# Optimization experiments

Measured on AMD Instinct MI355X. Metric: run time of the kernel, lower is better.

The kernel has to match this reference:

```python
import jax, jax.numpy as jnp
import numpy as np

N_HEAD = 16
N_EMBD = 1024
BLOCK = 2048
B, T = 4, 2048


def setup_inputs() -> dict:
    key = jax.random.key(0)
    ks = jax.random.split(key, 5)
    s = 0.02
    return {
        "x": jax.random.normal(ks[0], (B, T, N_EMBD), dtype=jnp.float32),
        "qkv_w": jax.random.normal(ks[1], (3 * N_EMBD, N_EMBD), dtype=jnp.float32) * s,
        "qkv_b": jnp.zeros((3 * N_EMBD,), dtype=jnp.float32),
        "proj_w": jax.random.normal(ks[2], (N_EMBD, N_EMBD), dtype=jnp.float32) * s,
        "proj_b": jnp.zeros((N_EMBD,), dtype=jnp.float32),
    }


def reference(x, qkv_w, qkv_b, proj_w, proj_b):
    Bx, Tx, C = x.shape
    hd = C // N_HEAD
    qkv = x @ qkv_w.T + qkv_b  # [B,T,3C]
    q, k, v = jnp.split(qkv, 3, axis=-1)
    # [B,T,C] -> [B,H,T,hd]
    def heads(t):
        return t.reshape(Bx, Tx, N_HEAD, hd).transpose(0, 2, 1, 3)
    q, k, v = heads(q), heads(k), heads(v)
    scores = jnp.einsum("bhqd,bhkd->bhqk", q, k) / jnp.sqrt(jnp.float32(hd))
    causal = jnp.tril(jnp.ones((Tx, Tx), dtype=bool))
    scores = jnp.where(causal[None, None, :, :], scores, -jnp.inf)
    attn = jax.nn.softmax(scores, axis=-1)
    out = jnp.einsum("bhqk,bhkd->bhqd", attn, v)
    out = out.transpose(0, 2, 1, 3).reshape(Bx, Tx, C)
    return out @ proj_w.T + proj_b
```

## Files before the change

kernel.cpp:

```cpp
#include <hip/hip_runtime.h>
#include <stdint.h>
#include <math.h>

#define DEVI __device__ __forceinline__

typedef __attribute__((ext_vector_type(8))) short bf16x8;
typedef __attribute__((ext_vector_type(4))) float f32x4;

DEVI unsigned short f2bf(float f) {
  union { float f; unsigned u; } v; v.f = f;
  unsigned u = v.u;
  u += 0x7fffu + ((u >> 16) & 1u);
  return (unsigned short)(u >> 16);
}

DEVI unsigned cvt_pk_bf16(float a, float b) {
  unsigned r;
  asm("v_cvt_pk_bf16_f32 %0, %1, %2" : "=v"(r) : "v"(a), "v"(b));
  return r;
}

DEVI f32x4 mfma16(bf16x8 a, bf16x8 b, f32x4 c) {
  return __builtin_amdgcn_mfma_f32_16x16x32_bf16(a, b, c, 0, 0, 0);
}

DEVI void gld16(const unsigned short* g, unsigned short* l) {
  __builtin_amdgcn_global_load_lds(
      (const __attribute__((address_space(1))) unsigned int*)(uintptr_t)g,
      (__attribute__((address_space(3))) unsigned int*)(unsigned int)(uintptr_t)l,
      16, 0, 0);
}

#define VMCNT(n) asm volatile("s_waitcnt vmcnt(" #n ")" ::: "memory")
#define BAR()                              \
  do {                                     \
    __builtin_amdgcn_s_barrier();          \
    __builtin_amdgcn_sched_barrier(0);     \
  } while (0)

__global__ __launch_bounds__(256) void cvt_kernel(const float* __restrict__ in,
                                                  unsigned short* __restrict__ out, int n) {
  int i = (blockIdx.x * 256 + threadIdx.x) * 4;
  if (i < n) {
    float4 v = *(const float4*)(in + i);
    unsigned lo = f2bf(v.x) | ((unsigned)f2bf(v.y) << 16);
    unsigned hi = f2bf(v.z) | ((unsigned)f2bf(v.w) << 16);
    uint2 o; o.x = lo; o.y = hi;
    *(uint2*)(out + i) = o;
  }
}

template <int MODE>
__global__ __launch_bounds__(512, 2) void gemm8(
    const unsigned short* __restrict__ A, const unsigned short* __restrict__ Bw,
    const float* __restrict__ bias, float* __restrict__ Cf,
    unsigned short* __restrict__ Qo, unsigned short* __restrict__ Ko,
    unsigned short* __restrict__ Vo, int M, int N, int K, int nbx) {
  extern __shared__ unsigned short lds[];
  const int tid = threadIdx.x;
  const int lane = tid & 63;
  const int w = tid >> 6;
  const int wm = w >> 2, wn = w & 3;
  const int lr = lane & 15, lq = lane >> 4;

  const int cpx = gridDim.x >> 3;
  const int swz = (blockIdx.x & 7) * cpx + (blockIdx.x >> 3);
  const int bx = swz % nbx, by = swz / nbx;
  const int m0 = by * 256, n0 = bx * 256;

  const int sr = lane >> 3;
  const int sc = ((lane & 7) ^ sr) << 3;
  const unsigned short* pa = A + (size_t)(m0 + sr) * K + sc;
  const unsigned short* pb = Bw + (size_t)(n0 + sr) * K + sc;

  const int aA0 = w, aA1 = 16 + w;
  const int aB0 = 8 + w, aB1 = 24 + w;
  const int bA0 = (w & 3) + ((w >> 2) << 3), bA1 = bA0 + 16;
  const int bB0 = bA0 + 4, bB1 = bA1 + 4;

  const int bs0 = (lq ^ (lr & 7)) << 3;
  const int bs1 = ((lq + 4) ^ (lr & 7)) << 3;

  f32x4 acc[8][4] = {};

  auto sA = [&](int buf, int kt, int c) {
    gld16(pa + (size_t)(c << 3) * K + kt, lds + buf * 32768 + (c << 9));
  };
  auto sB = [&](int buf, int kt, int c) {
    gld16(pb + (size_t)(c << 3) * K + kt, lds + buf * 32768 + 16384 + (c << 9));
  };

#define PH(buf, mh, nh)                                                          \
  {                                                                              \
    const unsigned short* As_ = lds + (buf) * 32768;                             \
    const unsigned short* Bs_ = As_ + 16384;                                     \
    bf16x8 a0[4], a1[4], b0[2], b1[2];                                           \
    _Pragma("unroll") for (int i = 0; i < 4; ++i) {                              \
      int ar = wm * 128 + (mh) * 64 + i * 16 + lr;                               \
      a0[i] = *(const bf16x8*)(As_ + ar * 64 + bs0);                             \
      a1[i] = *(const bf16x8*)(As_ + ar * 64 + bs1);                             \
    }                                                                            \
    _Pragma("unroll") for (int j = 0; j < 2; ++j) {                              \
      int br = wn * 64 + (nh) * 32 + j * 16 + lr;                                \
      b0[j] = *(const bf16x8*)(Bs_ + br * 64 + bs0);                             \
      b1[j] = *(const bf16x8*)(Bs_ + br * 64 + bs1);                             \
    }                                                                            \
    __builtin_amdgcn_s_setprio(1);                                               \
    _Pragma("unroll") for (int i = 0; i < 4; ++i)                                \
      _Pragma("unroll") for (int j = 0; j < 2; ++j) {                            \
        acc[(mh) * 4 + i][(nh) * 2 + j] =                                        \
            mfma16(a0[i], b0[j], acc[(mh) * 4 + i][(nh) * 2 + j]);               \
        acc[(mh) * 4 + i][(nh) * 2 + j] =                                        \
            mfma16(a1[i], b1[j], acc[(mh) * 4 + i][(nh) * 2 + j]);               \
      }                                                                          \
    __builtin_amdgcn_s_setprio(0);                                               \
  }

  sA(0, 0, aA0); sA(0, 0, aA1);
  sB(0, 0, bA0); sB(0, 0, bA1);
  sB(0, 0, bB0); sB(0, 0, bB1);
  sA(0, 0, aB0); sA(0, 0, aB1);
  VMCNT(4);
  BAR();

  const int NT = K >> 6;
  for (int t = 0; t < NT - 1; ++t) {
    const int buf = t & 1, nb = buf ^ 1;
    const int kt = (t + 1) << 6;
    sA(nb, kt, aA0); sA(nb, kt, aA1);
    PH(buf, 0, 0);
    VMCNT(4); BAR();
    sB(nb, kt, bA0); sB(nb, kt, bA1);
    PH(buf, 0, 1);
    VMCNT(4); BAR();
    sB(nb, kt, bB0); sB(nb, kt, bB1);
    PH(buf, 1, 0);
    sA(nb, kt, aB0); sA(nb, kt, aB1);
    PH(buf, 1, 1);
    VMCNT(4); BAR();
  }
  {
    const int buf = (NT - 1) & 1;
    PH(buf, 0, 0);
    VMCNT(2); BAR();
    PH(buf, 0, 1);
    VMCNT(0); BAR();
    PH(buf, 1, 0);
    PH(buf, 1, 1);
  }
#undef PH

#pragma unroll
  for (int mt = 0; mt < 8; ++mt) {
#pragma unroll
    for (int nt = 0; nt < 4; ++nt) {
      int n_g = n0 + wn * 64 + nt * 16 + lr;
      float bv = bias[n_g];
      if (MODE == 1) {
#pragma unroll
        for (int r = 0; r < 4; ++r) {
          int m_g = m0 + wm * 128 + mt * 16 + lq * 4 + r;
          Cf[(size_t)m_g * N + n_g] = acc[mt][nt][r] + bv;
        }
      } else {
        int which = n_g >> 10;
        int rem = n_g & 1023;
        int h = rem >> 6, d = rem & 63;
        int m_base = m0 + wm * 128 + mt * 16 + lq * 4;
        int b = m_base >> 11, tt = m_base & 2047;
        if (which == 2) {
          uint2 pv;
          pv.x = cvt_pk_bf16(acc[mt][nt][0] + bv, acc[mt][nt][1] + bv);
          pv.y = cvt_pk_bf16(acc[mt][nt][2] + bv, acc[mt][nt][3] + bv);
          *(uint2*)(Vo + (((size_t)(b * 16 + h) * 64 + d) * 2048 + tt)) = pv;
        } else {
          unsigned short* p = (which == 0) ? Qo : Ko;
#pragma unroll
          for (int r = 0; r < 4; ++r) {
            size_t idx = (((size_t)(b * 16 + h) * 2048) + tt + r) * 64 + d;
            p[idx] = f2bf(acc[mt][nt][r] + bv);
          }
        }
      }
    }
  }
}

__global__ __launch_bounds__(512, 4) void attn_kernel(
    const unsigned short* __restrict__ Q, const unsigned short* __restrict__ K,
    const unsigned short* __restrict__ V, unsigned short* __restrict__ Y) {
  constexpr int T = 2048, HD = 64, H = 16;
  __shared__ unsigned short Kt[2][64 * 72];
  __shared__ unsigned short Vt[2][64 * 72];
  __shared__ unsigned short Pt[8][16 * 72];

  const int tid = threadIdx.x;
  const int lane = tid & 63;
  const int w = tid >> 6;
  const int lr = lane & 15, lq = lane >> 4;
  const int pair = blockIdx.x;
  const int h = blockIdx.y;
  const int b = blockIdx.z;
  const size_t bh = (size_t)(b * H + h) * T * HD;
  const float SC = 0.125f * 1.44269504089f;

  const int krow = tid >> 3, kcb = (tid & 7) << 3;

  float4 kr, vr;
  auto load_tile = [&](int jt) {
    const int c0 = jt * 64;
    kr = *(const float4*)(K + bh + (size_t)(c0 + krow) * HD + kcb);
    vr = *(const float4*)(V + bh + (size_t)krow * T + c0 + kcb);
  };
  auto stage = [&](int buf) {
    *(float4*)(&Kt[buf][krow * 72 + kcb]) = kr;
    *(float4*)(&Vt[buf][krow * 72 + kcb]) = vr;
  };

  load_tile(0);

  for (int phase = 0; phase < 2; ++phase) {
    const int qt = phase ? (15 - pair) : pair;
    const int q0 = qt * 128;
    const int nkv = 2 * qt + 2;
    const int qmin = q0 + w * 16;
    const int qmax = qmin + 15;

    bf16x8 qf[2];
#pragma unroll
    for (int kb = 0; kb < 2; ++kb)
      qf[kb] = *(const bf16x8*)(Q + bh + (size_t)(qmin + lr) * HD + kb * 32 + lq * 8);

    f32x4 o[4] = {};
    float mi = -INFINITY, li = 0.f;

    stage(0);
    load_tile(1);
    __syncthreads();

    for (int jt = 0; jt < nkv; ++jt) {
      const int c0 = jt * 64;
      const int buf = jt & 1;

      if (c0 <= qmax) {
        f32x4 s[4];
        __builtin_amdgcn_s_setprio(1);
#pragma unroll
        for (int nt = 0; nt < 4; ++nt) {
          bf16x8 kf0 = *(const bf16x8*)(&Kt[buf][(nt * 16 + lr) * 72 + lq * 8]);
          bf16x8 kf1 = *(const bf16x8*)(&Kt[buf][(nt * 16 + lr) * 72 + 32 + lq * 8]);
          f32x4 z = {};
          z = mfma16(kf0, qf[0], z);
          s[nt] = mfma16(kf1, qf[1], z);
        }
        __builtin_amdgcn_s_setprio(0);
        if (c0 + 63 > qmin) {
          int qg = qmin + lr;
#pragma unroll
          for (int nt = 0; nt < 4; ++nt)
#pragma unroll
            for (int r = 0; r < 4; ++r) {
              int kvg = c0 + nt * 16 + lq * 4 + r;
              if (kvg > qg) s[nt][r] = -INFINITY;
            }
        }
        float mx = -INFINITY;
#pragma unroll
        for (int nt = 0; nt < 4; ++nt)
          mx = fmaxf(mx, fmaxf(fmaxf(s[nt][0], s[nt][1]),
                               fmaxf(s[nt][2], s[nt][3])));
        mx = fmaxf(mx, __shfl_xor(mx, 16));
        mx = fmaxf(mx, __shfl_xor(mx, 32));
        float mxs = mx * SC;
        if (!__all(mxs <= mi + 8.f)) {
          float mnew = fmaxf(mi, mxs);
          float alpha = __builtin_amdgcn_exp2f(mi - mnew);
          mi = mnew;
          li *= alpha;
#pragma unroll
          for (int nt = 0; nt < 4; ++nt)
#pragma unroll
            for (int r = 0; r < 4; ++r) o[nt][r] *= alpha;
        }
        float rs = 0.f;
#pragma unroll
        for (int nt = 0; nt < 4; ++nt) {
          float p0 = __builtin_amdgcn_exp2f(fmaf(s[nt][0], SC, -mi));
          float p1 = __builtin_amdgcn_exp2f(fmaf(s[nt][1], SC, -mi));
          float p2 = __builtin_amdgcn_exp2f(fmaf(s[nt][2], SC, -mi));
          float p3 = __builtin_amdgcn_exp2f(fmaf(s[nt][3], SC, -mi));
          rs += (p0 + p1) + (p2 + p3);
          uint2 pk;
          pk.x = cvt_pk_bf16(p0, p1);
          pk.y = cvt_pk_bf16(p2, p3);
          *(uint2*)(&Pt[w][lr * 72 + nt * 16 + lq * 4]) = pk;
        }
        li += rs;
        bf16x8 pf[2];
#pragma unroll
        for (int kb = 0; kb < 2; ++kb)
          pf[kb] = *(const bf16x8*)(&Pt[w][lr * 72 + kb * 32 + lq * 8]);
        __builtin_amdgcn_s_setprio(1);
#pragma unroll
        for (int nt = 0; nt < 4; ++nt) {
          bf16x8 vf0 = *(const bf16x8*)(&Vt[buf][(nt * 16 + lr) * 72 + lq * 8]);
          bf16x8 vf1 = *(const bf16x8*)(&Vt[buf][(nt * 16 + lr) * 72 + 32 + lq * 8]);
          o[nt] = mfma16(vf0, pf[0], o[nt]);
          o[nt] = mfma16(vf1, pf[1], o[nt]);
        }
        __builtin_amdgcn_s_setprio(0);
      }

      if (jt + 1 < nkv) {
        stage(buf ^ 1);
        if (jt + 2 < nkv) load_tile(jt + 2);
        else if (phase == 0) load_tile(0);
        __syncthreads();
      }
    }

    {
      li += __shfl_xor(li, 16);
      li += __shfl_xor(li, 32);
      float inv = 1.f / li;
      int t_g = qmin + lr;
#pragma unroll
      for (int nt = 0; nt < 4; ++nt) {
        uint2 yv;
        yv.x = cvt_pk_bf16(o[nt][0] * inv, o[nt][1] * inv);
        yv.y = cvt_pk_bf16(o[nt][2] * inv, o[nt][3] * inv);
        *(uint2*)(Y + ((size_t)(b * T + t_g)) * 1024 + h * 64 + nt * 16 + lq * 4) = yv;
      }
    }
  }
}

extern "C" void kernel_launch(void* const* d_in, const int* in_sizes, int n_in,
                              void* d_out, int out_size, void* d_ws, size_t ws_size,
                              hipStream_t stream) {
  const float* x = (const float*)d_in[0];
  const float* qkv_w = (const float*)d_in[1];
  const float* qkv_b = (const float*)d_in[2];
  const float* proj_w = (const float*)d_in[3];
  const float* proj_b = (const float*)d_in[4];
  float* out = (float*)d_out;

  unsigned short* ws = (unsigned short*)d_ws;
  unsigned short* xb = ws;
  unsigned short* wqkv = xb + 8388608;
  unsigned short* wproj = wqkv + 3145728;
  unsigned short* Qb = wproj + 1048576;
  unsigned short* Kb = Qb + 8388608;
  unsigned short* Vb = Kb + 8388608;
  unsigned short* Yb = Vb + 8388608;

  auto* g0 = gemm8<0>;
  auto* g1 = gemm8<1>;
  static bool attr_set = false;
  if (!attr_set) {
    (void)hipFuncSetAttribute((const void*)g0,
                              hipFuncAttributeMaxDynamicSharedMemorySize, 131072);
    (void)hipFuncSetAttribute((const void*)g1,
                              hipFuncAttributeMaxDynamicSharedMemorySize, 131072);
    attr_set = true;
  }

  cvt_kernel<<<8388608 / 1024, 256, 0, stream>>>(x, xb, 8388608);
  cvt_kernel<<<3145728 / 1024, 256, 0, stream>>>(qkv_w, wqkv, 3145728);
  cvt_kernel<<<1048576 / 1024, 256, 0, stream>>>(proj_w, wproj, 1048576);

  gemm8<0><<<dim3(384), 512, 131072, stream>>>(xb, wqkv, qkv_b, nullptr, Qb, Kb, Vb,
                                               8192, 3072, 1024, 12);
  attn_kernel<<<dim3(8, 16, 4), 512, 0, stream>>>(Qb, Kb, Vb, Yb);
  gemm8<1><<<dim3(128), 512, 131072, stream>>>(Yb, wproj, proj_b, out, nullptr, nullptr,
                                               nullptr, 8192, 1024, 1024, 4);
}
```

Baseline: 257.6 us.

## Process two query sub-tiles per wave in attention and merge conversion kernels

The attention kernel now gives each wave 32 query rows (two 16-row sub-tiles) instead of 16. Each K/V fragment read from LDS therefore feeds twice as many MFMAs, and the grid is halved to 4x16x4 blocks covering 256-row query tiles. Launch bounds drop to 2 blocks per CU because register use roughly doubles, and fewer, larger blocks may hurt causal load balance and occupancy. The three fp32-to-bf16 conversion launches are also merged into one kernel that picks its source by block index, saving two launches.

```diff
diff --git a/kernel.cpp b/kernel.cpp
--- a/kernel.cpp
+++ b/kernel.cpp
@@ -38,16 +38,21 @@
     __builtin_amdgcn_sched_barrier(0);     \
   } while (0)
 
-__global__ __launch_bounds__(256) void cvt_kernel(const float* __restrict__ in,
-                                                  unsigned short* __restrict__ out, int n) {
-  int i = (blockIdx.x * 256 + threadIdx.x) * 4;
-  if (i < n) {
-    float4 v = *(const float4*)(in + i);
-    unsigned lo = f2bf(v.x) | ((unsigned)f2bf(v.y) << 16);
-    unsigned hi = f2bf(v.z) | ((unsigned)f2bf(v.w) << 16);
-    uint2 o; o.x = lo; o.y = hi;
-    *(uint2*)(out + i) = o;
-  }
+__global__ __launch_bounds__(256) void cvt3_kernel(
+    const float* __restrict__ a, unsigned short* __restrict__ oa,
+    const float* __restrict__ b, unsigned short* __restrict__ ob,
+    const float* __restrict__ c, unsigned short* __restrict__ oc) {
+  int bid = blockIdx.x;
+  const float* in; unsigned short* out; int i;
+  if (bid < 8192)       { in = a; out = oa; i = bid; }
+  else if (bid < 11264) { in = b; out = ob; i = bid - 8192; }
+  else                  { in = c; out = oc; i = bid - 11264; }
+  int idx = (i * 256 + (int)threadIdx.x) * 4;
+  float4 v = *(const float4*)(in + idx);
+  unsigned lo = f2bf(v.x) | ((unsigned)f2bf(v.y) << 16);
+  unsigned hi = f2bf(v.z) | ((unsigned)f2bf(v.w) << 16);
+  uint2 o; o.x = lo; o.y = hi;
+  *(uint2*)(out + idx) = o;
 }
 
 template <int MODE>
@@ -186,7 +191,7 @@
   }
 }
 
-__global__ __launch_bounds__(512, 4) void attn_kernel(
+__global__ __launch_bounds__(512, 2) void attn_kernel(
     const unsigned short* __restrict__ Q, const unsigned short* __restrict__ K,
     const unsigned short* __restrict__ V, unsigned short* __restrict__ Y) {
   constexpr int T = 2048, HD = 64, H = 16;
@@ -220,19 +225,21 @@
   load_tile(0);
 
   for (int phase = 0; phase < 2; ++phase) {
-    const int qt = phase ? (15 - pair) : pair;
-    const int q0 = qt * 128;
-    const int nkv = 2 * qt + 2;
-    const int qmin = q0 + w * 16;
-    const int qmax = qmin + 15;
-
-    bf16x8 qf[2];
-#pragma unroll
-    for (int kb = 0; kb < 2; ++kb)
-      qf[kb] = *(const bf16x8*)(Q + bh + (size_t)(qmin + lr) * HD + kb * 32 + lq * 8);
-
-    f32x4 o[4] = {};
-    float mi = -INFINITY, li = 0.f;
+    const int qt = phase ? (7 - pair) : pair;
+    const int q0 = qt * 256;
+    const int nkv = 4 * (qt + 1);
+    const int qw = q0 + w * 32;
+
+    bf16x8 qf[2][2];
+#pragma unroll
+    for (int qs = 0; qs < 2; ++qs)
+#pragma unroll
+      for (int kb = 0; kb < 2; ++kb)
+        qf[qs][kb] = *(const bf16x8*)(Q + bh + (size_t)(qw + qs * 16 + lr) * HD +
+                                      kb * 32 + lq * 8);
+
+    f32x4 o[2][4] = {};
+    float mi[2] = {-INFINITY, -INFINITY}, li[2] = {0.f, 0.f};
 
     stage(0);
     load_tile(1);
@@ -242,71 +249,90 @@
       const int c0 = jt * 64;
       const int buf = jt & 1;
 
-      if (c0 <= qmax) {
-        f32x4 s[4];
+      if (c0 <= qw + 31) {
+        f32x4 s[2][4];
         __builtin_amdgcn_s_setprio(1);
 #pragma unroll
         for (int nt = 0; nt < 4; ++nt) {
           bf16x8 kf0 = *(const bf16x8*)(&Kt[buf][(nt * 16 + lr) * 72 + lq * 8]);
           bf16x8 kf1 = *(const bf16x8*)(&Kt[buf][(nt * 16 + lr) * 72 + 32 + lq * 8]);
-          f32x4 z = {};
-          z = mfma16(kf0, qf[0], z);
-          s[nt] = mfma16(kf1, qf[1], z);
+#pragma unroll
+          for (int qs = 0; qs < 2; ++qs) {
+            f32x4 z = {};
+            z = mfma16(kf0, qf[qs][0], z);
+            s[qs][nt] = mfma16(kf1, qf[qs][1], z);
+          }
         }
         __builtin_amdgcn_s_setprio(0);
-        if (c0 + 63 > qmin) {
-          int qg = qmin + lr;
+        if (c0 + 63 > qw) {
+#pragma unroll
+          for (int qs = 0; qs < 2; ++qs) {
+            int qg = qw + qs * 16 + lr;
+#pragma unroll
+            for (int nt = 0; nt < 4; ++nt)
+#pragma unroll
+              for (int r = 0; r < 4; ++r) {
+                int kvg = c0 + nt * 16 + lq * 4 + r;
+                if (kvg > qg) s[qs][nt][r] = -INFINITY;
+              }
+          }
+        }
+        float mxs[2];
+#pragma unroll
+        for (int qs = 0; qs < 2; ++qs) {
+          float mx = -INFINITY;
 #pragma unroll
           for (int nt = 0; nt < 4; ++nt)
-#pragma unroll
-            for (int r = 0; r < 4; ++r) {
-              int kvg = c0 + nt * 16 + lq * 4 + r;
-              if (kvg > qg) s[nt][r] = -INFINITY;
-            }
-        }
-        float mx = -INFINITY;
-#pragma unroll
-        for (int nt = 0; nt < 4; ++nt)
-          mx = fmaxf(mx, fmaxf(fmaxf(s[nt][0], s[nt][1]),
-                               fmaxf(s[nt][2], s[nt][3])));
-        mx = fmaxf(mx, __shfl_xor(mx, 16));
-        mx = fmaxf(mx, __shfl_xor(mx, 32));
-        float mxs = mx * SC;
-        if (!__all(mxs <= mi + 8.f)) {
-          float mnew = fmaxf(mi, mxs);
-          float alpha = __builtin_amdgcn_exp2f(mi - mnew);
-          mi = mnew;
-          li *= alpha;
-#pragma unroll
-          for (int nt = 0; nt < 4; ++nt)
-#pragma unroll
-            for (int r = 0; r < 4; ++r) o[nt][r] *= alpha;
-        }
-        float rs = 0.f;
-#pragma unroll
-        for (int nt = 0; nt < 4; ++nt) {
-          float p0 = __builtin_amdgcn_exp2f(fmaf(s[nt][0], SC, -mi));
-          float p1 = __builtin_amdgcn_exp2f(fmaf(s[nt][1], SC, -mi));
-          float p2 = __builtin_amdgcn_exp2f(fmaf(s[nt][2], SC, -mi));
-          float p3 = __builtin_amdgcn_exp2f(fmaf(s[nt][3], SC, -mi));
-          rs += (p0 + p1) + (p2 + p3);
-          uint2 pk;
-          pk.x = cvt_pk_bf16(p0, p1);
-          pk.y = cvt_pk_bf16(p2, p3);
-          *(uint2*)(&Pt[w][lr * 72 + nt * 16 + lq * 4]) = pk;
-        }
-        li += rs;
-        bf16x8 pf[2];
-#pragma unroll
-        for (int kb = 0; kb < 2; ++kb)
-          pf[kb] = *(const bf16x8*)(&Pt[w][lr * 72 + kb * 32 + lq * 8]);
+            mx = fmaxf(mx, fmaxf(fmaxf(s[qs][nt][0], s[qs][nt][1]),
+                                 fmaxf(s[qs][nt][2], s[qs][nt][3])));
+          mx = fmaxf(mx, __shfl_xor(mx, 16));
+          mx = fmaxf(mx, __shfl_xor(mx, 32));
+          mxs[qs] = mx * SC;
+        }
+        if (!__all((mxs[0] <= mi[0] + 8.f) && (mxs[1] <= mi[1] + 8.f))) {
+#pragma unroll
+          for (int qs = 0; qs < 2; ++qs) {
+            float mnew = fmaxf(mi[qs], mxs[qs]);
+            float alpha = __builtin_amdgcn_exp2f(mi[qs] - mnew);
+            mi[qs] = mnew;
+            li[qs] *= alpha;
+#pragma unroll
+            for (int nt = 0; nt < 4; ++nt)
+#pragma unroll
+              for (int r = 0; r < 4; ++r) o[qs][nt][r] *= alpha;
+          }
+        }
+        bf16x8 pf[2][2];
+#pragma unroll
+        for (int qs = 0; qs < 2; ++qs) {
+          float rs = 0.f;
+#pragma unroll
+          for (int nt = 0; nt < 4; ++nt) {
+            float p0 = __builtin_amdgcn_exp2f(fmaf(s[qs][nt][0], SC, -mi[qs]));
+            float p1 = __builtin_amdgcn_exp2f(fmaf(s[qs][nt][1], SC, -mi[qs]));
+            float p2 = __builtin_amdgcn_exp2f(fmaf(s[qs][nt][2], SC, -mi[qs]));
+            float p3 = __builtin_amdgcn_exp2f(fmaf(s[qs][nt][3], SC, -mi[qs]));
+            rs += (p0 + p1) + (p2 + p3);
+            uint2 pk;
+            pk.x = cvt_pk_bf16(p0, p1);
+            pk.y = cvt_pk_bf16(p2, p3);
+            *(uint2*)(&Pt[w][lr * 72 + nt * 16 + lq * 4]) = pk;
+          }
+          li[qs] += rs;
+#pragma unroll
+          for (int kb = 0; kb < 2; ++kb)
+            pf[qs][kb] = *(const bf16x8*)(&Pt[w][lr * 72 + kb * 32 + lq * 8]);
+        }
         __builtin_amdgcn_s_setprio(1);
 #pragma unroll
         for (int nt = 0; nt < 4; ++nt) {
           bf16x8 vf0 = *(const bf16x8*)(&Vt[buf][(nt * 16 + lr) * 72 + lq * 8]);
           bf16x8 vf1 = *(const bf16x8*)(&Vt[buf][(nt * 16 + lr) * 72 + 32 + lq * 8]);
-          o[nt] = mfma16(vf0, pf[0], o[nt]);
-          o[nt] = mfma16(vf1, pf[1], o[nt]);
+#pragma unroll
+          for (int qs = 0; qs < 2; ++qs) {
+            o[qs][nt] = mfma16(vf0, pf[qs][0], o[qs][nt]);
+            o[qs][nt] = mfma16(vf1, pf[qs][1], o[qs][nt]);
+          }
         }
         __builtin_amdgcn_s_setprio(0);
       }
@@ -319,16 +345,18 @@
       }
     }
 
-    {
-      li += __shfl_xor(li, 16);
-      li += __shfl_xor(li, 32);
-      float inv = 1.f / li;
-      int t_g = qmin + lr;
+#pragma unroll
+    for (int qs = 0; qs < 2; ++qs) {
+      float l = li[qs];
+      l += __shfl_xor(l, 16);
+      l += __shfl_xor(l, 32);
+      float inv = 1.f / l;
+      int t_g = qw + qs * 16 + lr;
 #pragma unroll
       for (int nt = 0; nt < 4; ++nt) {
         uint2 yv;
-        yv.x = cvt_pk_bf16(o[nt][0] * inv, o[nt][1] * inv);
-        yv.y = cvt_pk_bf16(o[nt][2] * inv, o[nt][3] * inv);
+        yv.x = cvt_pk_bf16(o[qs][nt][0] * inv, o[qs][nt][1] * inv);
+        yv.y = cvt_pk_bf16(o[qs][nt][2] * inv, o[qs][nt][3] * inv);
         *(uint2*)(Y + ((size_t)(b * T + t_g)) * 1024 + h * 64 + nt * 16 + lq * 4) = yv;
       }
     }
@@ -365,13 +393,11 @@
     attr_set = true;
   }
 
-  cvt_kernel<<<8388608 / 1024, 256, 0, stream>>>(x, xb, 8388608);
-  cvt_kernel<<<3145728 / 1024, 256, 0, stream>>>(qkv_w, wqkv, 3145728);
-  cvt_kernel<<<1048576 / 1024, 256, 0, stream>>>(proj_w, wproj, 1048576);
+  cvt3_kernel<<<12288, 256, 0, stream>>>(x, xb, qkv_w, wqkv, proj_w, wproj);
 
   gemm8<0><<<dim3(384), 512, 131072, stream>>>(xb, wqkv, qkv_b, nullptr, Qb, Kb, Vb,
                                                8192, 3072, 1024, 12);
-  attn_kernel<<<dim3(8, 16, 4), 512, 0, stream>>>(Qb, Kb, Vb, Yb);
+  attn_kernel<<<dim3(4, 16, 4), 512, 0, stream>>>(Qb, Kb, Vb, Yb);
   gemm8<1><<<dim3(128), 512, 131072, stream>>>(Yb, wproj, proj_b, out, nullptr, nullptr,
                                                nullptr, 8192, 1024, 1024, 4);
 }
```

Result: no change. 256.6 us (-0.4%).
